# Optimization experiments

Hardware: AMD Instinct MI355X
Metric: run time of the kernel (lower is better)

Reference implementation:

```python
import jax, jax.numpy as jnp
import numpy as np

NUM_HEADS = 32
KV_HEADS = 8
HEAD_DIM = 128
ROPE_BASE = 10000.0

def apply_rope(x):
    # x: [B, H, S, D]
    B, H, S, D = x.shape
    inv_freq = 1.0 / (ROPE_BASE ** (jnp.arange(0, D, 2, dtype=jnp.float32) / D))  # [D/2]
    t = jnp.arange(S, dtype=jnp.float32)
    freqs = jnp.einsum('s,d->sd', t, inv_freq)                 # [S, D/2]
    emb = jnp.concatenate([freqs, freqs], axis=-1)             # [S, D]
    cos = jnp.cos(emb)[None, None, :, :].astype(x.dtype)
    sin = jnp.sin(emb)[None, None, :, :].astype(x.dtype)
    x1, x2 = x[..., : D // 2], x[..., D // 2 :]
    rotated = jnp.concatenate([-x2, x1], axis=-1)
    return x * cos + rotated * sin

def setup_inputs() -> dict:
    key = jax.random.key(0)
    ks = jax.random.split(key, 6)
    B, S, H = 1, 2048, 4096
    scale = 1.0 / np.sqrt(H)
    return {
        'hidden_states': jax.random.normal(ks[0], (B, S, H), jnp.float32),
        'attention_mask': jnp.zeros((B, S), jnp.float32),
        'Wq': jax.random.normal(ks[1], (H, NUM_HEADS * HEAD_DIM), jnp.float32) * scale,
        'Wk': jax.random.normal(ks[2], (H, KV_HEADS * HEAD_DIM), jnp.float32) * scale,
        'Wv': jax.random.normal(ks[3], (H, KV_HEADS * HEAD_DIM), jnp.float32) * scale,
        'Wo': jax.random.normal(ks[4], (NUM_HEADS * HEAD_DIM, H), jnp.float32) * scale,
    }

def reference(hidden_states, attention_mask, Wq, Wk, Wv, Wo):
    B, S, _ = hidden_states.shape
    groups = NUM_HEADS // KV_HEADS
    q = (hidden_states @ Wq).reshape(B, S, NUM_HEADS, HEAD_DIM).transpose(0, 2, 1, 3)  # [B,H,S,D]
    k = (hidden_states @ Wk).reshape(B, S, KV_HEADS, HEAD_DIM).transpose(0, 2, 1, 3)   # [B,KV,S,D]
    v = (hidden_states @ Wv).reshape(B, S, KV_HEADS, HEAD_DIM).transpose(0, 2, 1, 3)
    q = apply_rope(q)
    k = apply_rope(k)
    # GQA: repeat kv heads to match query heads
    k = jnp.repeat(k, groups, axis=1)  # [B,H,S,D]
    v = jnp.repeat(v, groups, axis=1)
    scale = 1.0 / jnp.sqrt(jnp.asarray(HEAD_DIM, q.dtype))
    scores = jnp.einsum('bhqd,bhkd->bhqk', q, k) * scale       # [B,H,S,S]
    scores = scores + attention_mask[:, None, None, :]
    attn = jax.nn.softmax(scores, axis=-1)
    out = jnp.einsum('bhqk,bhkd->bhqd', attn, v)               # [B,H,S,D]
    out = out.transpose(0, 2, 1, 3).reshape(B, S, NUM_HEADS * HEAD_DIM)
    return out @ Wo
```

## Files before the change

kernel.cpp:

```cpp
#include <hip/hip_runtime.h>
#include <hip/hip_bf16.h>

typedef __bf16 bf16_t;
typedef __bf16 bf16x8 __attribute__((ext_vector_type(8)));
typedef __bf16 bf16x4 __attribute__((ext_vector_type(4)));
typedef float f32x4 __attribute__((ext_vector_type(4)));
typedef float f32x16 __attribute__((ext_vector_type(16)));

#define LOG2E 1.4426950408889634f

__device__ __forceinline__ void gload_lds16(const void* g, void* l) {
  __builtin_amdgcn_global_load_lds((const __attribute__((address_space(1))) void*)g,
                                   (__attribute__((address_space(3))) void*)l, 16, 0, 0);
}

__device__ __forceinline__ unsigned pk_bf16(float a, float b) {
  unsigned r;
  asm("v_cvt_pk_bf16_f32 %0, %1, %2" : "=v"(r) : "v"(a), "v"(b));
  return r;
}

__device__ __forceinline__ void trcvt_body(const float* src, bf16_t* dst, int R,
                                           int C, int cx, int cy, int tx, int ty,
                                           float (*tile)[33], bool perm) {
  int c0 = cx * 32, r0 = cy * 32;
#pragma unroll
  for (int i = 0; i < 4; ++i)
    tile[ty + i * 8][tx] = src[(size_t)(r0 + ty + i * 8) * C + c0 + tx];
  __syncthreads();
#pragma unroll
  for (int i = 0; i < 4; ++i) {
    int rc = c0 + ty + i * 8;
    int r_out = rc;
    if (perm) {
      int dd = rc & 127;
      int q = (dd & 15) + (dd & 16) + (((dd >> 5) & 1) ? 64 : 0) + ((dd >> 6) ? 32 : 0);
      r_out = (rc & ~127) | q;
    }
    dst[(size_t)r_out * R + r0 + tx] = (bf16_t)tile[tx][ty + i * 8];
  }
}

__global__ __launch_bounds__(256) void prep_kernel(
    const float* __restrict__ hidden, const float* __restrict__ Wq,
    const float* __restrict__ Wk, const float* __restrict__ Wv,
    const float* __restrict__ Wo, bf16_t* __restrict__ hB,
    bf16_t* __restrict__ Wqt, bf16_t* __restrict__ Wkvt,
    bf16_t* __restrict__ Wot, float* __restrict__ cosT,
    float* __restrict__ sinT) {
  __shared__ float tile[32][33];
  const int bx = blockIdx.x;
  const int t = threadIdx.x;
  const int tx = t & 31, ty = t >> 5;
  if (bx < 4096) {
    int i = bx * 256 + t;
    const float4* s4 = (const float4*)hidden;
    float4 a = s4[2 * i], b = s4[2 * i + 1];
    bf16x8 o;
    o[0] = (bf16_t)a.x; o[1] = (bf16_t)a.y; o[2] = (bf16_t)a.z; o[3] = (bf16_t)a.w;
    o[4] = (bf16_t)b.x; o[5] = (bf16_t)b.y; o[6] = (bf16_t)b.z; o[7] = (bf16_t)b.w;
    *(bf16x8*)(hB + 8 * (size_t)i) = o;
  } else if (bx < 4608) {
    int i = (bx - 4096) * 256 + t;
    int s = i >> 6, d = i & 63;
    float ang = (float)s * powf(10000.0f, -(float)d * (1.0f / 64.0f));
    cosT[i] = cosf(ang);
    sinT[i] = sinf(ang);
  } else if (bx < 20992) {
    int j = bx - 4608;
    trcvt_body(Wq, Wqt, 4096, 4096, j % 128, j / 128, tx, ty, tile, true);
  } else if (bx < 25088) {
    int j = bx - 20992;
    trcvt_body(Wk, Wkvt, 4096, 1024, j % 32, j / 32, tx, ty, tile, true);
  } else if (bx < 29184) {
    int j = bx - 25088;
    trcvt_body(Wv, Wkvt + (size_t)1024 * 4096, 4096, 1024, j % 32, j / 32, tx, ty, tile, false);
  } else {
    int j = bx - 29184;
    trcvt_body(Wo, Wot, 4096, 4096, j % 128, j / 128, tx, ty, tile, false);
  }
}

__global__ __launch_bounds__(256) void trb_kernel(const bf16_t* __restrict__ src,
                                                  bf16_t* __restrict__ dst, int R, int C) {
  __shared__ bf16_t tile[32][33];
  int c0 = blockIdx.x * 32, r0 = blockIdx.y * 32;
  int tx = threadIdx.x, ty = threadIdx.y;
#pragma unroll
  for (int i = 0; i < 4; ++i)
    tile[ty + i * 8][tx] = src[(size_t)(r0 + ty + i * 8) * C + c0 + tx];
  __syncthreads();
#pragma unroll
  for (int i = 0; i < 4; ++i)
    dst[(size_t)(c0 + ty + i * 8) * R + r0 + tx] = tile[tx][ty + i * 8];
}

__global__ __launch_bounds__(512, 2) void proj_gemm_kernel(
    const bf16_t* __restrict__ A, const bf16_t* __restrict__ Wqt,
    const bf16_t* __restrict__ Wkvt, const float* __restrict__ cosT,
    const float* __restrict__ sinT, bf16_t* __restrict__ Qb,
    bf16_t* __restrict__ Kb, bf16_t* __restrict__ Vb) {
  constexpr int K = 4096;
  extern __shared__ unsigned char sMem[];
  const int bx = blockIdx.x;
  const int mt = bx & 7, nt = bx >> 3;
  const int bm = mt * 256;
  const bf16_t* Btb = (nt < 16) ? (Wqt + (size_t)nt * 256 * K)
                                : (Wkvt + (size_t)(nt - 16) * 256 * K);

  const int t = threadIdx.x;
  const int rowU = t >> 2;
  const int cole = ((t & 3) * 8) ^ ((rowU & 8) ? 16 : 0);
  const bf16_t* aS = A + (size_t)(bm + rowU) * K + cole;
  const bf16_t* bS = Btb + (size_t)rowU * K + cole;

  const int lane = t & 63, w = t >> 6;
  const int wm = w >> 2, wn = w & 3;
  const int lr = lane & 15, lq = lane >> 4;
  const int colb = (lq * 16) ^ ((lr & 8) ? 32 : 0);

  auto stA = [&](int c, int h, int j) {
    unsigned char* d = sMem + c * 65536 + h * 16384 + t * 16;
    const bf16_t* g = aS + (size_t)h * 128 * K + j * 64;
    gload_lds16(g, d);
    gload_lds16(g + 32, d + 8192);
  };
  auto stB = [&](int c, int h, int j) {
    unsigned char* d = sMem + c * 65536 + 32768 + h * 16384 + t * 16;
    const bf16_t* g = bS + (size_t)h * 128 * K + j * 64;
    gload_lds16(g, d);
    gload_lds16(g + 32, d + 8192);
  };
  auto LA = [&](int c, int half, int mi, int kk) {
    return *(const bf16x8*)(sMem + c * 65536 + wm * 16384 + kk * 8192 +
                            (half * 64 + mi * 16 + lr) * 64 + colb);
  };
  auto LB = [&](int c, int ni, int kk) {
    return *(const bf16x8*)(sMem + c * 65536 + 32768 + (wn >> 1) * 16384 + kk * 8192 +
                            ((wn & 1) * 64 + ni * 16 + lr) * 64 + colb);
  };

  f32x4 acc[8][4];
#pragma unroll
  for (int i = 0; i < 8; ++i)
#pragma unroll
    for (int n = 0; n < 4; ++n) acc[i][n] = f32x4{0.f, 0.f, 0.f, 0.f};

  stA(0, 0, 0); stA(0, 1, 0); stB(0, 0, 0); stB(0, 1, 0);
  stB(1, 0, 1); stB(1, 1, 1);
  asm volatile("s_waitcnt vmcnt(4)" ::: "memory");
  __builtin_amdgcn_s_barrier();
  __builtin_amdgcn_sched_barrier(0);

  bf16x8 af[4][2], bf[2][2], bf2[2][2];
  for (int j = 0; j < 64; ++j) {
    const int c = j & 1, cn = c ^ 1;
    const int jp1 = (j + 1 < 64) ? j + 1 : 63;
    const int jp2 = (j + 2 < 64) ? j + 2 : 63;
#pragma unroll
    for (int mi = 0; mi < 4; ++mi)
#pragma unroll
      for (int kk = 0; kk < 2; ++kk) af[mi][kk] = LA(c, 0, mi, kk);
#pragma unroll
    for (int ni = 0; ni < 2; ++ni)
#pragma unroll
      for (int kk = 0; kk < 2; ++kk) bf[ni][kk] = LB(c, ni, kk);
    stA(cn, 0, jp1);
    __builtin_amdgcn_s_barrier();
    __builtin_amdgcn_sched_barrier(0);
    __builtin_amdgcn_s_setprio(1);
#pragma unroll
    for (int kk = 0; kk < 2; ++kk)
#pragma unroll
      for (int mi = 0; mi < 4; ++mi)
#pragma unroll
        for (int ni = 0; ni < 2; ++ni)
          acc[mi][ni] = __builtin_amdgcn_mfma_f32_16x16x32_bf16(af[mi][kk], bf[ni][kk],
                                                                acc[mi][ni], 0, 0, 0);
    __builtin_amdgcn_s_setprio(0);
    __builtin_amdgcn_sched_barrier(0);
    __builtin_amdgcn_s_barrier();
#pragma unroll
    for (int ni = 0; ni < 2; ++ni)
#pragma unroll
      for (int kk = 0; kk < 2; ++kk) bf2[ni][kk] = LB(c, 2 + ni, kk);
    stA(cn, 1, jp1);
    __builtin_amdgcn_s_barrier();
    __builtin_amdgcn_sched_barrier(0);
    __builtin_amdgcn_s_setprio(1);
#pragma unroll
    for (int kk = 0; kk < 2; ++kk)
#pragma unroll
      for (int mi = 0; mi < 4; ++mi)
#pragma unroll
        for (int ni = 0; ni < 2; ++ni)
          acc[mi][2 + ni] = __builtin_amdgcn_mfma_f32_16x16x32_bf16(af[mi][kk], bf2[ni][kk],
                                                                    acc[mi][2 + ni], 0, 0, 0);
    __builtin_amdgcn_s_setprio(0);
    __builtin_amdgcn_sched_barrier(0);
    __builtin_amdgcn_s_barrier();
#pragma unroll
    for (int mi = 0; mi < 4; ++mi)
#pragma unroll
      for (int kk = 0; kk < 2; ++kk) af[mi][kk] = LA(c, 1, mi, kk);
    stB(c, 0, jp2);
    __builtin_amdgcn_s_barrier();
    __builtin_amdgcn_sched_barrier(0);
    __builtin_amdgcn_s_setprio(1);
#pragma unroll
    for (int kk = 0; kk < 2; ++kk)
#pragma unroll
      for (int mi = 0; mi < 4; ++mi)
#pragma unroll
        for (int ni = 0; ni < 2; ++ni)
          acc[4 + mi][2 + ni] = __builtin_amdgcn_mfma_f32_16x16x32_bf16(
              af[mi][kk], bf2[ni][kk], acc[4 + mi][2 + ni], 0, 0, 0);
    __builtin_amdgcn_s_setprio(0);
    __builtin_amdgcn_sched_barrier(0);
    __builtin_amdgcn_s_barrier();
    stB(c, 1, jp2);
    __builtin_amdgcn_sched_barrier(0);
    __builtin_amdgcn_s_setprio(1);
#pragma unroll
    for (int kk = 0; kk < 2; ++kk)
#pragma unroll
      for (int mi = 0; mi < 4; ++mi)
#pragma unroll
        for (int ni = 0; ni < 2; ++ni)
          acc[4 + mi][ni] = __builtin_amdgcn_mfma_f32_16x16x32_bf16(
              af[mi][kk], bf[ni][kk], acc[4 + mi][ni], 0, 0, 0);
    __builtin_amdgcn_s_setprio(0);
    asm volatile("s_waitcnt vmcnt(4)" ::: "memory");
    __builtin_amdgcn_sched_barrier(0);
    __builtin_amdgcn_s_barrier();
  }

  if (nt < 20) {
    const bool isQ = nt < 16;
    bf16_t* dst = isQ ? Qb : Kb;
    const int ld = isQ ? 4096 : 1024;
    const int hh = isQ ? (nt * 2 + (wn >> 1)) : ((nt - 16) * 2 + (wn >> 1));
    const float qs = isQ ? 0.12751743f : 1.0f;
    const int dbase = lr + 32 * (wn & 1);
#pragma unroll
    for (int half = 0; half < 2; ++half)
#pragma unroll
      for (int mi = 0; mi < 4; ++mi)
#pragma unroll
        for (int ni = 0; ni < 2; ++ni) {
          int d = dbase + 16 * ni;
#pragma unroll
          for (int r = 0; r < 4; ++r) {
            int srow = bm + wm * 128 + half * 64 + mi * 16 + lq * 4 + r;
            float cv = cosT[srow * 64 + d], sv = sinT[srow * 64 + d];
            float x1 = acc[half * 4 + mi][ni][r], x2 = acc[half * 4 + mi][ni + 2][r];
            dst[(size_t)srow * ld + hh * 128 + d] = (bf16_t)((x1 * cv - x2 * sv) * qs);
            dst[(size_t)srow * ld + hh * 128 + d + 64] = (bf16_t)((x2 * cv + x1 * sv) * qs);
          }
        }
  } else {
    const int col0 = (nt - 20) * 256 + wn * 64;
#pragma unroll
    for (int half = 0; half < 2; ++half)
#pragma unroll
      for (int mi = 0; mi < 4; ++mi)
#pragma unroll
        for (int ni = 0; ni < 4; ++ni)
#pragma unroll
          for (int r = 0; r < 4; ++r) {
            int srow = bm + wm * 128 + half * 64 + mi * 16 + lq * 4 + r;
            Vb[(size_t)srow * 1024 + col0 + ni * 16 + lr] =
                (bf16_t)acc[half * 4 + mi][ni][r];
          }
  }
}

__global__ __launch_bounds__(256, 2) void out_gemm_kernel(
    const bf16_t* __restrict__ A, const bf16_t* __restrict__ B0,
    float* __restrict__ Cout) {
  constexpr int K = 4096;
  constexpr int MT = 16;
  __shared__ alignas(16) unsigned char sAB[32768];
  unsigned char* sA = sAB;
  unsigned char* sB = sAB + 16384;
  const int bx = blockIdx.x;
  const int mt = bx % MT, nt = bx / MT;
  const int bm = mt * 128;
  const bf16_t* Bt = B0 + (size_t)nt * 128 * K;

  const int t = threadIdx.x;
  const int sr = t >> 3;
  const int scol = ((t & 7) ^ (sr & 7)) * 8;
  const bf16_t* aG = A + (size_t)(bm + sr) * K + scol;
  const bf16_t* bG = Bt + (size_t)sr * K + scol;
  unsigned char* aL = sA + t * 16;
  unsigned char* bL = sB + t * 16;

  const int lane = t & 63, w = t >> 6;
  const int lr = lane & 15, lq = lane >> 4;
  const int swz = (lr & 7) << 4;

  f32x4 acc[2][8];
#pragma unroll
  for (int m = 0; m < 2; ++m)
#pragma unroll
    for (int n = 0; n < 8; ++n) acc[m][n] = f32x4{0.f, 0.f, 0.f, 0.f};

  for (int k0 = 0; k0 < K; k0 += 64) {
    __syncthreads();
#pragma unroll
    for (int p = 0; p < 4; ++p) {
      gload_lds16(aG + (size_t)(p * 32) * K + k0, aL + p * 4096);
      gload_lds16(bG + (size_t)(p * 32) * K + k0, bL + p * 4096);
    }
    __syncthreads();
#pragma unroll
    for (int kk = 0; kk < 2; ++kk) {
      bf16x8 af[2], bfr[8];
#pragma unroll
      for (int m = 0; m < 2; ++m)
        af[m] = *(const bf16x8*)(sA + (w * 32 + m * 16 + lr) * 128 +
                                 ((kk * 64 + lq * 16) ^ swz));
#pragma unroll
      for (int n = 0; n < 8; ++n)
        bfr[n] = *(const bf16x8*)(sB + (n * 16 + lr) * 128 +
                                  ((kk * 64 + lq * 16) ^ swz));
#pragma unroll
      for (int m = 0; m < 2; ++m)
#pragma unroll
        for (int n = 0; n < 8; ++n)
          acc[m][n] = __builtin_amdgcn_mfma_f32_16x16x32_bf16(af[m], bfr[n],
                                                              acc[m][n], 0, 0, 0);
    }
  }
#pragma unroll
  for (int m = 0; m < 2; ++m)
#pragma unroll
    for (int n = 0; n < 8; ++n)
#pragma unroll
      for (int r = 0; r < 4; ++r)
        Cout[(size_t)(bm + w * 32 + m * 16 + lq * 4 + r) * 4096 + nt * 128 +
             n * 16 + lr] = acc[m][n][r];
}

__global__ __launch_bounds__(256, 2) void attn_kernel(
    const bf16_t* __restrict__ Qb, const bf16_t* __restrict__ Kb,
    const bf16_t* __restrict__ Vt, const float* __restrict__ mask,
    bf16_t* __restrict__ Ob) {
  extern __shared__ unsigned char sMem[];
  const int bx = blockIdx.x;
  const int h = bx >> 4, qt = bx & 15;
  const int kvh = h >> 2;
  const int t = threadIdx.x, lane = t & 63, w = t >> 6;
  const int ln = lane & 31, hi = lane >> 5;
  const int q0 = qt * 128 + w * 32;
  const int swz = (ln & 7) << 4;

  bf16x8 qf[8];
#pragma unroll
  for (int ds = 0; ds < 8; ++ds)
    qf[ds] = *(const bf16x8*)(Qb + (size_t)(q0 + ln) * 4096 + h * 128 + ds * 16 + hi * 8);

  const int krow = t >> 4, kg = t & 15;
  const bf16_t* kSrc = Kb + (size_t)krow * 1024 + kvh * 128 +
                       (((kg * 16) ^ ((krow & 7) << 4)) >> 1);
  const int vrow = t >> 3, vg = t & 7;
  const bf16_t* vSrc = Vt + (size_t)(kvh * 128 + vrow) * 2048 +
                       (((vg * 16) ^ ((vrow & 7) << 4)) >> 1);

  auto stage = [&](int c, int kt) {
    unsigned char* kD = sMem + c * 16384 + t * 16;
    unsigned char* vD = sMem + 32768 + c * 16384 + t * 16;
#pragma unroll
    for (int p = 0; p < 4; ++p)
      gload_lds16(kSrc + (size_t)(kt * 64 + p * 16) * 1024, kD + p * 4096);
#pragma unroll
    for (int p = 0; p < 4; ++p)
      gload_lds16(vSrc + (size_t)(p * 32) * 2048 + kt * 64, vD + p * 4096);
    if (t < 16) gload_lds16(mask + kt * 64 + t * 4, sMem + 65536 + c * 256 + t * 16);
  };

  f32x16 o[4];
#pragma unroll
  for (int db = 0; db < 4; ++db)
#pragma unroll
    for (int e = 0; e < 16; ++e) o[db][e] = 0.f;
  float mrun = -1e30f, lp = 0.f;

  stage(0, 0);
  __syncthreads();

  for (int kt = 0; kt < 32; ++kt) {
    const int c = kt & 1;
    if (kt < 31) stage(c ^ 1, kt + 1);
    const unsigned char* sK = sMem + c * 16384;
    const unsigned char* sV = sMem + 32768 + c * 16384;
    const unsigned char* sMk = sMem + 65536 + c * 256;

#pragma unroll
    for (int sub = 0; sub < 2; ++sub) {
      f32x16 s;
#pragma unroll
      for (int e = 0; e < 16; ++e) s[e] = 0.f;
      __builtin_amdgcn_s_setprio(1);
#pragma unroll
      for (int ds = 0; ds < 8; ++ds) {
        bf16x8 kf = *(const bf16x8*)(sK + (sub * 32 + ln) * 256 +
                                     ((ds * 32 + hi * 16) ^ swz));
        s = __builtin_amdgcn_mfma_f32_32x32x16_bf16(kf, qf[ds], s, 0, 0, 0);
      }
      __builtin_amdgcn_s_setprio(0);
#pragma unroll
      for (int rg = 0; rg < 4; ++rg) {
        float4 mv = *(const float4*)(sMk + (sub * 32 + rg * 8 + 4 * hi) * 4);
        s[rg * 4 + 0] += LOG2E * mv.x; s[rg * 4 + 1] += LOG2E * mv.y;
        s[rg * 4 + 2] += LOG2E * mv.z; s[rg * 4 + 3] += LOG2E * mv.w;
      }
      float pm = s[0];
#pragma unroll
      for (int e = 1; e < 16; ++e) pm = fmaxf(pm, s[e]);
      pm = fmaxf(pm, __shfl_xor(pm, 32));
      if (!__all(pm - mrun <= 11.5f)) {
        float nm = fmaxf(mrun, pm);
        float al = exp2f(mrun - nm);
        mrun = nm;
        lp *= al;
#pragma unroll
        for (int db = 0; db < 4; ++db)
#pragma unroll
          for (int e = 0; e < 16; ++e) o[db][e] *= al;
      }
      float p[16], ps = 0.f;
#pragma unroll
      for (int e = 0; e < 16; ++e) {
        p[e] = exp2f(s[e] - mrun);
        ps += p[e];
      }
      lp += ps;
#pragma unroll
      for (int hh = 0; hh < 2; ++hh) {
        unsigned w0 = pk_bf16(p[8 * hh + 0], p[8 * hh + 1]);
        unsigned w1 = pk_bf16(p[8 * hh + 2], p[8 * hh + 3]);
        unsigned w2 = pk_bf16(p[8 * hh + 4], p[8 * hh + 5]);
        unsigned w3 = pk_bf16(p[8 * hh + 6], p[8 * hh + 7]);
        unsigned pw0 = __shfl_xor((int)w0, 32), pw1 = __shfl_xor((int)w1, 32);
        unsigned pw2 = __shfl_xor((int)w2, 32), pw3 = __shfl_xor((int)w3, 32);
        union { unsigned u[4]; bf16x8 v; } pf;
        pf.u[0] = hi ? pw2 : w0;
        pf.u[1] = hi ? pw3 : w1;
        pf.u[2] = hi ? w2 : pw0;
        pf.u[3] = hi ? w3 : pw1;
        __builtin_amdgcn_s_setprio(1);
#pragma unroll
        for (int db = 0; db < 4; ++db) {
          bf16x8 vf = *(const bf16x8*)(sV + (db * 32 + ln) * 128 +
                                       ((sub * 64 + hh * 32 + hi * 16) ^ swz));
          o[db] = __builtin_amdgcn_mfma_f32_32x32x16_bf16(vf, pf.v, o[db], 0, 0, 0);
        }
        __builtin_amdgcn_s_setprio(0);
      }
    }
    __syncthreads();
  }

  float l = lp + __shfl_xor(lp, 32);
  float inv = 1.0f / l;
  bf16_t* orow = Ob + (size_t)(q0 + ln) * 4096 + h * 128;
#pragma unroll
  for (int db = 0; db < 4; ++db)
#pragma unroll
    for (int rg = 0; rg < 4; ++rg) {
      bf16x4 ov;
#pragma unroll
      for (int j = 0; j < 4; ++j) ov[j] = (bf16_t)(o[db][rg * 4 + j] * inv);
      *(bf16x4*)(orow + db * 32 + rg * 8 + hi * 4) = ov;
    }
}

extern "C" void kernel_launch(void* const* d_in, const int* in_sizes, int n_in,
                              void* d_out, int out_size, void* d_ws, size_t ws_size,
                              hipStream_t stream) {
  const float* hidden = (const float*)d_in[0];
  const float* mask = (const float*)d_in[1];
  const float* Wq = (const float*)d_in[2];
  const float* Wk = (const float*)d_in[3];
  const float* Wv = (const float*)d_in[4];
  const float* Wo = (const float*)d_in[5];
  float* out = (float*)d_out;
  char* ws = (char*)d_ws;

  bf16_t* hB   = (bf16_t*)(ws + 0);
  bf16_t* Wqt  = (bf16_t*)(ws + 16777216);
  bf16_t* Wkvt = (bf16_t*)(ws + 50331648);
  bf16_t* Wot  = (bf16_t*)(ws + 67108864);
  bf16_t* Qb   = (bf16_t*)(ws + 100663296);
  bf16_t* Kb   = (bf16_t*)(ws + 117440512);
  bf16_t* Vb   = (bf16_t*)(ws + 121634816);
  bf16_t* Vt   = (bf16_t*)(ws + 125829120);
  bf16_t* Ob   = (bf16_t*)(ws + 130023424);
  float*  cosT = (float*)(ws + 146800640);
  float*  sinT = (float*)(ws + 147324928);

  hipFuncSetAttribute((const void*)attn_kernel,
                      hipFuncAttributeMaxDynamicSharedMemorySize, 66560);
  hipFuncSetAttribute((const void*)proj_gemm_kernel,
                      hipFuncAttributeMaxDynamicSharedMemorySize, 131072);

  prep_kernel<<<45568, 256, 0, stream>>>(hidden, Wq, Wk, Wv, Wo, hB, Wqt, Wkvt,
                                         Wot, cosT, sinT);
  proj_gemm_kernel<<<192, 512, 131072, stream>>>(hB, Wqt, Wkvt, cosT, sinT, Qb, Kb, Vb);
  trb_kernel<<<dim3(32, 64), dim3(32, 8), 0, stream>>>(Vb, Vt, 2048, 1024);
  attn_kernel<<<512, 256, 66560, stream>>>(Qb, Kb, Vt, mask, Ob);
  out_gemm_kernel<<<512, 256, 0, stream>>>(Ob, Wot, out);
}
```

Baseline: 333.8 us.

## Enlarge out-proj GEMM tiles with pipelined 8-wave schedule; widen attention blocks to 512 threads

The output projection GEMM moves from 128x128 tiles with 4 waves to 256x128 tiles with 8 waves. It double-buffers A and B in LDS, overlaps loads with MFMA phases using barriers, sched_barrier and setprio, and uses a new XOR swizzle. The attention kernel now runs 256 blocks of 512 threads, each covering 256 query rows, so every staged K/V tile is shared by twice as many queries. Both changes aim to raise data reuse and overlap memory with compute. The cost is a heavier LDS footprint, more register pressure, and only 256 blocks to fill the device.

```diff
diff --git a/kernel.cpp b/kernel.cpp
--- a/kernel.cpp
+++ b/kernel.cpp
@@ -275,85 +275,154 @@
   }
 }
 
-__global__ __launch_bounds__(256, 2) void out_gemm_kernel(
+__global__ __launch_bounds__(512, 2) void out_gemm_kernel(
     const bf16_t* __restrict__ A, const bf16_t* __restrict__ B0,
     float* __restrict__ Cout) {
   constexpr int K = 4096;
-  constexpr int MT = 16;
-  __shared__ alignas(16) unsigned char sAB[32768];
-  unsigned char* sA = sAB;
-  unsigned char* sB = sAB + 16384;
+  extern __shared__ unsigned char sMem[];
   const int bx = blockIdx.x;
-  const int mt = bx % MT, nt = bx / MT;
-  const int bm = mt * 128;
+  const int mt = bx & 7, nt = bx >> 3;
+  const int bm = mt * 256;
   const bf16_t* Bt = B0 + (size_t)nt * 128 * K;
 
   const int t = threadIdx.x;
-  const int sr = t >> 3;
-  const int scol = ((t & 7) ^ (sr & 7)) * 8;
-  const bf16_t* aG = A + (size_t)(bm + sr) * K + scol;
-  const bf16_t* bG = Bt + (size_t)sr * K + scol;
-  unsigned char* aL = sA + t * 16;
-  unsigned char* bL = sB + t * 16;
+  const int rowU = t >> 2;
+  const int cole = ((t & 3) * 8) ^ ((rowU & 8) ? 16 : 0);
+  const bf16_t* aS = A + (size_t)(bm + rowU) * K + cole;
+  const bf16_t* bS = Bt + (size_t)rowU * K + cole;
 
   const int lane = t & 63, w = t >> 6;
+  const int wm = w >> 2, wn = w & 3;
   const int lr = lane & 15, lq = lane >> 4;
-  const int swz = (lr & 7) << 4;
-
-  f32x4 acc[2][8];
-#pragma unroll
-  for (int m = 0; m < 2; ++m)
-#pragma unroll
-    for (int n = 0; n < 8; ++n) acc[m][n] = f32x4{0.f, 0.f, 0.f, 0.f};
-
-  for (int k0 = 0; k0 < K; k0 += 64) {
-    __syncthreads();
-#pragma unroll
-    for (int p = 0; p < 4; ++p) {
-      gload_lds16(aG + (size_t)(p * 32) * K + k0, aL + p * 4096);
-      gload_lds16(bG + (size_t)(p * 32) * K + k0, bL + p * 4096);
-    }
-    __syncthreads();
-#pragma unroll
-    for (int kk = 0; kk < 2; ++kk) {
-      bf16x8 af[2], bfr[8];
-#pragma unroll
-      for (int m = 0; m < 2; ++m)
-        af[m] = *(const bf16x8*)(sA + (w * 32 + m * 16 + lr) * 128 +
-                                 ((kk * 64 + lq * 16) ^ swz));
-#pragma unroll
-      for (int n = 0; n < 8; ++n)
-        bfr[n] = *(const bf16x8*)(sB + (n * 16 + lr) * 128 +
-                                  ((kk * 64 + lq * 16) ^ swz));
-#pragma unroll
-      for (int m = 0; m < 2; ++m)
-#pragma unroll
-        for (int n = 0; n < 8; ++n)
-          acc[m][n] = __builtin_amdgcn_mfma_f32_16x16x32_bf16(af[m], bfr[n],
-                                                              acc[m][n], 0, 0, 0);
-    }
+  const int colb = (lq * 16) ^ ((lr & 8) ? 32 : 0);
+
+  auto stA = [&](int c, int h, int j) {
+    unsigned char* d = sMem + c * 49152 + h * 16384 + t * 16;
+    const bf16_t* g = aS + (size_t)h * 128 * K + j * 64;
+    gload_lds16(g, d);
+    gload_lds16(g + 32, d + 8192);
+  };
+  auto stB = [&](int c, int j) {
+    unsigned char* d = sMem + c * 49152 + 32768 + t * 16;
+    const bf16_t* g = bS + j * 64;
+    gload_lds16(g, d);
+    gload_lds16(g + 32, d + 8192);
+  };
+  auto LA = [&](int c, int half, int mi, int kk) {
+    return *(const bf16x8*)(sMem + c * 49152 + wm * 16384 + kk * 8192 +
+                            (half * 64 + mi * 16 + lr) * 64 + colb);
+  };
+  auto LB = [&](int c, int ni, int kk) {
+    return *(const bf16x8*)(sMem + c * 49152 + 32768 + kk * 8192 +
+                            (wn * 32 + ni * 16 + lr) * 64 + colb);
+  };
+
+  f32x4 acc[8][2];
+#pragma unroll
+  for (int i = 0; i < 8; ++i)
+#pragma unroll
+    for (int n = 0; n < 2; ++n) acc[i][n] = f32x4{0.f, 0.f, 0.f, 0.f};
+
+  stA(0, 0, 0); stA(0, 1, 0); stB(0, 0);
+  stB(1, 1);
+  asm volatile("s_waitcnt vmcnt(2)" ::: "memory");
+  __builtin_amdgcn_s_barrier();
+  __builtin_amdgcn_sched_barrier(0);
+
+  bf16x8 af[4][2], bf0[2], bf1[2];
+  for (int j = 0; j < 64; ++j) {
+    const int c = j & 1, cn = c ^ 1;
+    const int jp1 = (j + 1 < 64) ? j + 1 : 63;
+    const int jp2 = (j + 2 < 64) ? j + 2 : 63;
+#pragma unroll
+    for (int mi = 0; mi < 4; ++mi)
+#pragma unroll
+      for (int kk = 0; kk < 2; ++kk) af[mi][kk] = LA(c, 0, mi, kk);
+#pragma unroll
+    for (int kk = 0; kk < 2; ++kk) bf0[kk] = LB(c, 0, kk);
+    stA(cn, 0, jp1);
+    __builtin_amdgcn_s_barrier();
+    __builtin_amdgcn_sched_barrier(0);
+    __builtin_amdgcn_s_setprio(1);
+#pragma unroll
+    for (int kk = 0; kk < 2; ++kk)
+#pragma unroll
+      for (int mi = 0; mi < 4; ++mi)
+        acc[mi][0] = __builtin_amdgcn_mfma_f32_16x16x32_bf16(af[mi][kk], bf0[kk],
+                                                             acc[mi][0], 0, 0, 0);
+    __builtin_amdgcn_s_setprio(0);
+    __builtin_amdgcn_sched_barrier(0);
+    __builtin_amdgcn_s_barrier();
+#pragma unroll
+    for (int kk = 0; kk < 2; ++kk) bf1[kk] = LB(c, 1, kk);
+    stA(cn, 1, jp1);
+    __builtin_amdgcn_s_barrier();
+    __builtin_amdgcn_sched_barrier(0);
+    __builtin_amdgcn_s_setprio(1);
+#pragma unroll
+    for (int kk = 0; kk < 2; ++kk)
+#pragma unroll
+      for (int mi = 0; mi < 4; ++mi)
+        acc[mi][1] = __builtin_amdgcn_mfma_f32_16x16x32_bf16(af[mi][kk], bf1[kk],
+                                                             acc[mi][1], 0, 0, 0);
+    __builtin_amdgcn_s_setprio(0);
+    __builtin_amdgcn_sched_barrier(0);
+    __builtin_amdgcn_s_barrier();
+#pragma unroll
+    for (int mi = 0; mi < 4; ++mi)
+#pragma unroll
+      for (int kk = 0; kk < 2; ++kk) af[mi][kk] = LA(c, 1, mi, kk);
+    stB(c, jp2);
+    __builtin_amdgcn_s_barrier();
+    __builtin_amdgcn_sched_barrier(0);
+    __builtin_amdgcn_s_setprio(1);
+#pragma unroll
+    for (int kk = 0; kk < 2; ++kk)
+#pragma unroll
+      for (int mi = 0; mi < 4; ++mi)
+        acc[4 + mi][1] = __builtin_amdgcn_mfma_f32_16x16x32_bf16(af[mi][kk], bf1[kk],
+                                                                 acc[4 + mi][1], 0, 0, 0);
+    __builtin_amdgcn_s_setprio(0);
+    __builtin_amdgcn_sched_barrier(0);
+    __builtin_amdgcn_s_barrier();
+    __builtin_amdgcn_s_setprio(1);
+#pragma unroll
+    for (int kk = 0; kk < 2; ++kk)
+#pragma unroll
+      for (int mi = 0; mi < 4; ++mi)
+        acc[4 + mi][0] = __builtin_amdgcn_mfma_f32_16x16x32_bf16(af[mi][kk], bf0[kk],
+                                                                 acc[4 + mi][0], 0, 0, 0);
+    __builtin_amdgcn_s_setprio(0);
+    asm volatile("s_waitcnt vmcnt(2)" ::: "memory");
+    __builtin_amdgcn_sched_barrier(0);
+    __builtin_amdgcn_s_barrier();
   }
-#pragma unroll
-  for (int m = 0; m < 2; ++m)
-#pragma unroll
-    for (int n = 0; n < 8; ++n)
-#pragma unroll
-      for (int r = 0; r < 4; ++r)
-        Cout[(size_t)(bm + w * 32 + m * 16 + lq * 4 + r) * 4096 + nt * 128 +
-             n * 16 + lr] = acc[m][n][r];
-}
-
-__global__ __launch_bounds__(256, 2) void attn_kernel(
+
+#pragma unroll
+  for (int half = 0; half < 2; ++half)
+#pragma unroll
+    for (int mi = 0; mi < 4; ++mi)
+#pragma unroll
+      for (int ni = 0; ni < 2; ++ni)
+#pragma unroll
+        for (int r = 0; r < 4; ++r) {
+          int row = bm + wm * 128 + half * 64 + mi * 16 + lq * 4 + r;
+          Cout[(size_t)row * 4096 + nt * 128 + wn * 32 + ni * 16 + lr] =
+              acc[half * 4 + mi][ni][r];
+        }
+}
+
+__global__ __launch_bounds__(512) void attn_kernel(
     const bf16_t* __restrict__ Qb, const bf16_t* __restrict__ Kb,
     const bf16_t* __restrict__ Vt, const float* __restrict__ mask,
     bf16_t* __restrict__ Ob) {
   extern __shared__ unsigned char sMem[];
   const int bx = blockIdx.x;
-  const int h = bx >> 4, qt = bx & 15;
+  const int h = bx >> 3, qt = bx & 7;
   const int kvh = h >> 2;
   const int t = threadIdx.x, lane = t & 63, w = t >> 6;
   const int ln = lane & 31, hi = lane >> 5;
-  const int q0 = qt * 128 + w * 32;
+  const int q0 = qt * 256 + w * 32;
   const int swz = (ln & 7) << 4;
 
   bf16x8 qf[8];
@@ -371,12 +440,10 @@
   auto stage = [&](int c, int kt) {
     unsigned char* kD = sMem + c * 16384 + t * 16;
     unsigned char* vD = sMem + 32768 + c * 16384 + t * 16;
-#pragma unroll
-    for (int p = 0; p < 4; ++p)
-      gload_lds16(kSrc + (size_t)(kt * 64 + p * 16) * 1024, kD + p * 4096);
-#pragma unroll
-    for (int p = 0; p < 4; ++p)
-      gload_lds16(vSrc + (size_t)(p * 32) * 2048 + kt * 64, vD + p * 4096);
+    gload_lds16(kSrc + (size_t)kt * 64 * 1024, kD);
+    gload_lds16(kSrc + (size_t)(kt * 64 + 32) * 1024, kD + 8192);
+    gload_lds16(vSrc + kt * 64, vD);
+    gload_lds16(vSrc + (size_t)64 * 2048 + kt * 64, vD + 8192);
     if (t < 16) gload_lds16(mask + kt * 64 + t * 4, sMem + 65536 + c * 256 + t * 16);
   };
 
@@ -505,11 +572,13 @@
                       hipFuncAttributeMaxDynamicSharedMemorySize, 66560);
   hipFuncSetAttribute((const void*)proj_gemm_kernel,
                       hipFuncAttributeMaxDynamicSharedMemorySize, 131072);
+  hipFuncSetAttribute((const void*)out_gemm_kernel,
+                      hipFuncAttributeMaxDynamicSharedMemorySize, 98304);
 
   prep_kernel<<<45568, 256, 0, stream>>>(hidden, Wq, Wk, Wv, Wo, hB, Wqt, Wkvt,
                                          Wot, cosT, sinT);
   proj_gemm_kernel<<<192, 512, 131072, stream>>>(hB, Wqt, Wkvt, cosT, sinT, Qb, Kb, Vb);
   trb_kernel<<<dim3(32, 64), dim3(32, 8), 0, stream>>>(Vb, Vt, 2048, 1024);
-  attn_kernel<<<512, 256, 66560, stream>>>(Qb, Kb, Vt, mask, Ob);
-  out_gemm_kernel<<<512, 256, 0, stream>>>(Ob, Wot, out);
-}
+  attn_kernel<<<256, 512, 66560, stream>>>(Qb, Kb, Vt, mask, Ob);
+  out_gemm_kernel<<<256, 512, 98304, stream>>>(Ob, Wot, out);
+}
```

New measurement: 327.4 us. Within noise of the previous version (-1.9%).
